# Kernel optimization log

Measured on AMD Instinct MI355X. Metric: run time of the kernel, lower is better.

The kernel has to match this reference:

```python
import math
import jax, jax.numpy as jnp
import numpy as np

D = 256       # d_model
R = 64        # low-rank bottleneck
E = 3         # num experts
KS = (1, 3, 5)
EPS = 0.1     # sinkhorn epsilon
ITERS = 10    # sinkhorn iterations


def _ln(x, g, b):
    m = jnp.mean(x, -1, keepdims=True)
    v = jnp.mean((x - m) ** 2, -1, keepdims=True)
    return (x - m) * jax.lax.rsqrt(v + 1e-5) * g + b


def _gelu(x):
    return jax.nn.gelu(x, approximate=False)  # torch nn.GELU default (erf)


def setup_inputs() -> dict:
    key = jax.random.key(0)
    ks = jax.random.split(key, 12)
    s = 0.02
    B, Lt, La = 16, 1024, 2048
    return {
        "text_feat": jax.random.normal(ks[0], (B, Lt, D), jnp.float32),
        "audio_feat": jax.random.normal(ks[1], (B, La, D), jnp.float32),
        # shared OT projection (LayerNorm + Linear, shared across modalities)
        "ln_g": jnp.ones((D,), jnp.float32),
        "ln_b": jnp.zeros((D,), jnp.float32),
        "W_sh": jax.random.normal(ks[2], (D, D), jnp.float32) * s,
        "b_sh": jnp.zeros((D,), jnp.float32),
        # contradiction router: Linear(d+1->d) GELU Linear(d->E)
        "Wr1": jax.random.normal(ks[3], (D, D + 1), jnp.float32) * s,
        "br1": jnp.zeros((D,), jnp.float32),
        "Wr2": jax.random.normal(ks[4], (E, D), jnp.float32) * s,
        "br2": jnp.zeros((E,), jnp.float32),
        # 3 low-rank conv experts (stacked where shapes match)
        "down_W": jax.random.normal(ks[5], (E, R, D), jnp.float32) * s,
        "down_b": jnp.zeros((E, R), jnp.float32),
        "conv_w1": jax.random.normal(ks[6], (R, R, 1), jnp.float32) * s,
        "conv_w3": jax.random.normal(ks[7], (R, R, 3), jnp.float32) * s,
        "conv_w5": jax.random.normal(ks[8], (R, R, 5), jnp.float32) * s,
        "conv_b": jnp.zeros((E, R), jnp.float32),
        "up_W": jax.random.normal(ks[9], (E, D, R), jnp.float32) * s,
        "up_b": jnp.zeros((E, D), jnp.float32),
        "en_g": jnp.ones((E, D), jnp.float32),
        "en_b": jnp.zeros((E, D), jnp.float32),
    }


def reference(text_feat, audio_feat, ln_g, ln_b, W_sh, b_sh, Wr1, br1, Wr2, br2,
              down_W, down_b, conv_w1, conv_w3, conv_w5, conv_b, up_W, up_b, en_g, en_b):
    B, Lt, _ = text_feat.shape
    La = audio_feat.shape[1]

    # ---- shared projection (dropout = identity at eval) ----
    Tp = _ln(text_feat, ln_g, ln_b) @ W_sh.T + b_sh      # [B,Lt,D]
    Ap = _ln(audio_feat, ln_g, ln_b) @ W_sh.T + b_sh     # [B,La,D]

    # ---- cosine cost ----
    Tn = Tp / jnp.maximum(jnp.linalg.norm(Tp, axis=-1, keepdims=True), 1e-12)
    An = Ap / jnp.maximum(jnp.linalg.norm(Ap, axis=-1, keepdims=True), 1e-12)
    cost = 1.0 - jnp.einsum('bmd,bnd->bmn', Tn, An)      # [B,Lt,La]

    # ---- log-domain Sinkhorn (uniform marginals, no masks) ----
    log_K = -cost / (EPS + 1e-8)
    log_mu = jnp.full((B, Lt), -math.log(Lt), jnp.float32)
    log_nu = jnp.full((B, La), -math.log(La), jnp.float32)
    lu = jnp.zeros((B, Lt), jnp.float32)
    lv = jnp.zeros((B, La), jnp.float32)
    for _ in range(ITERS):
        lu = log_mu - jax.scipy.special.logsumexp(log_K + lv[:, None, :], axis=-1)
        lu = jnp.nan_to_num(jnp.clip(lu, -1e9, 1e9), nan=0.0, posinf=1e9, neginf=-1e9)
        lv = log_nu - jax.scipy.special.logsumexp(log_K + lu[:, :, None], axis=1)
        lv = jnp.nan_to_num(jnp.clip(lv, -1e9, 1e9), nan=0.0, posinf=1e9, neginf=-1e9)
    pi = jnp.exp(lu[:, :, None] + log_K + lv[:, None, :])
    pi = jnp.nan_to_num(pi, nan=0.0, posinf=1.0, neginf=0.0)  # [B,Lt,La]

    A_al = jnp.einsum('bmn,bnd->bmd', pi, Ap)            # [B,Lt,D]
    S = jnp.sum(Tp * A_al, -1)                           # [B,Lt]
    resid = jnp.abs(Tp - A_al)                           # [B,Lt,D]

    # ---- contradiction router ----
    rin = jnp.concatenate([S[..., None], resid], -1)     # [B,Lt,D+1]
    G = jax.nn.softmax(_gelu(rin @ Wr1.T + br1) @ Wr2.T + br2, axis=-1)  # [B,Lt,E]

    # ---- multi-scale low-rank conv MoE over contradiction residual ----
    convs = (conv_w1, conv_w3, conv_w5)
    x = resid
    out = jnp.zeros_like(Tp)
    for e in range(E):
        h = _gelu(x @ down_W[e].T + down_b[e])           # [B,Lt,R]
        k = convs[e].shape[-1]
        pad = (k - 1) // 2
        hc = jax.lax.conv_general_dilated(
            h.transpose(0, 2, 1), convs[e], (1,), [(pad, pad)],
            dimension_numbers=('NCH', 'OIH', 'NCH')) + conv_b[e][None, :, None]
        h = _gelu(hc).transpose(0, 2, 1)                 # [B,Lt,R]
        h = h @ up_W[e].T + up_b[e]                      # [B,Lt,D]
        eo = _ln(h + x, en_g[e], en_b[e])
        out = out + G[..., e:e + 1] * eo
    return out
```

## Files before the change

### kernel.cpp

```cpp
#include <hip/hip_runtime.h>
#include <cstdio>

#define D_ 256
#define LT 1024
#define LA 2048
#define NB 16
#define RR_ 64
#define NRT (NB*LT)
#define NRA (NB*LA)

#define DECQ (-0.080645161f)

typedef short bf16x8 __attribute__((ext_vector_type(8)));
typedef float f32x4 __attribute__((ext_vector_type(4)));

__device__ __forceinline__ float gelu_f(float x) {
    return 0.5f * x * (1.0f + erff(x * 0.70710678118654752f));
}
__device__ __forceinline__ unsigned short f2bf(float f) {
    union { float f; unsigned int i; } c; c.f = f;
    unsigned int x = c.i;
    return (unsigned short)((x + 0x7fffu + ((x >> 16) & 1u)) >> 16);
}

__global__ __launch_bounds__(256) void k_prep_all(
    const float* __restrict__ W_sh, const float* __restrict__ down_W,
    const float* __restrict__ up_W, const float* __restrict__ Wr1,
    unsigned short* __restrict__ Wb, unsigned short* __restrict__ dWb,
    unsigned short* __restrict__ uWb, unsigned short* __restrict__ Wr1b)
{
    int i = blockIdx.x * 256 + threadIdx.x;
    if (i < 65536) Wb[i] = f2bf(W_sh[i]);
    else if (i < 114688) { int j = i - 65536; dWb[j] = f2bf(down_W[j]); }
    else if (i < 163840) { int j = i - 114688; uWb[j] = f2bf(up_W[j]); }
    else { int j = i - 163840; int n = j >> 8, k = j & 255; Wr1b[j] = f2bf(Wr1[(long)n * 257 + 1 + k]); }
}

__global__ __launch_bounds__(256) void k_lnproj_mfma(
    const float* __restrict__ X, const float* __restrict__ g, const float* __restrict__ bln,
    const unsigned short* __restrict__ Wb, const float* __restrict__ bsh,
    float* __restrict__ Pf, unsigned short* __restrict__ Nb)
{
    __shared__ short xb[64][264];
    __shared__ short Bs[256][40];
    int tid = threadIdx.x;
    long row0 = (long)blockIdx.x * 64;
    {
        int lane = tid & 31, rg = tid >> 5;
        float4 ga = *(const float4*)(g + lane * 8);
        float4 gb2 = *(const float4*)(g + lane * 8 + 4);
        float4 ba = *(const float4*)(bln + lane * 8);
        float4 bb2 = *(const float4*)(bln + lane * 8 + 4);
        for (int it = 0; it < 8; it++) {
            int r = it * 8 + rg;
            const float4* xp4 = (const float4*)(X + (row0 + r) * D_);
            float4 a = xp4[lane * 2], b = xp4[lane * 2 + 1];
            float s = a.x + a.y + a.z + a.w + b.x + b.y + b.z + b.w;
#pragma unroll
            for (int off = 16; off >= 1; off >>= 1) s += __shfl_xor(s, off);
            float mean = s * (1.0f / 256.0f);
            float q = (a.x - mean) * (a.x - mean) + (a.y - mean) * (a.y - mean)
                    + (a.z - mean) * (a.z - mean) + (a.w - mean) * (a.w - mean)
                    + (b.x - mean) * (b.x - mean) + (b.y - mean) * (b.y - mean)
                    + (b.z - mean) * (b.z - mean) + (b.w - mean) * (b.w - mean);
#pragma unroll
            for (int off = 16; off >= 1; off >>= 1) q += __shfl_xor(q, off);
            float ivar = rsqrtf(q * (1.0f / 256.0f) + 1e-5f);
            unsigned int u0 = f2bf((a.x - mean) * ivar * ga.x + ba.x);
            unsigned int u1 = f2bf((a.y - mean) * ivar * ga.y + ba.y);
            unsigned int u2 = f2bf((a.z - mean) * ivar * ga.z + ba.z);
            unsigned int u3 = f2bf((a.w - mean) * ivar * ga.w + ba.w);
            unsigned int u4 = f2bf((b.x - mean) * ivar * gb2.x + bb2.x);
            unsigned int u5 = f2bf((b.y - mean) * ivar * gb2.y + bb2.y);
            unsigned int u6 = f2bf((b.z - mean) * ivar * gb2.z + bb2.z);
            unsigned int u7 = f2bf((b.w - mean) * ivar * gb2.w + bb2.w);
            int4 pv;
            pv.x = (int)(u0 | (u1 << 16)); pv.y = (int)(u2 | (u3 << 16));
            pv.z = (int)(u4 | (u5 << 16)); pv.w = (int)(u6 | (u7 << 16));
            *(int4*)&xb[r][lane * 8] = pv;
        }
    }
    __syncthreads();
    int wid = tid >> 6, lane = tid & 63;
    int l15 = lane & 15, kq = lane >> 4;
    int m_local = wid * 16;
    f32x4 acc[16];
#pragma unroll
    for (int j = 0; j < 16; j++) acc[j] = (f32x4){0.f, 0.f, 0.f, 0.f};
    for (int kt = 0; kt < 8; kt++) {
        int k0 = kt * 32;
#pragma unroll
        for (int h = 0; h < 4; h++) {
            int idx = tid + 256 * h;
            int n = idx >> 2, qc = idx & 3;
            *(int4*)&Bs[n][qc * 8] = *(const int4*)(Wb + (long)n * D_ + k0 + qc * 8);
        }
        __syncthreads();
        bf16x8 af = *(const bf16x8*)&xb[m_local + l15][k0 + kq * 8];
#pragma unroll
        for (int j = 0; j < 16; j++) {
            bf16x8 bf = *(const bf16x8*)&Bs[j * 16 + l15][kq * 8];
            acc[j] = __builtin_amdgcn_mfma_f32_16x16x32_bf16(af, bf, acc[j], 0, 0, 0);
        }
        __syncthreads();
    }
#pragma unroll
    for (int j = 0; j < 16; j++) {
        float bv = bsh[j * 16 + l15];
#pragma unroll
        for (int r = 0; r < 4; r++) acc[j][r] += bv;
    }
    float sq[4] = {0.f, 0.f, 0.f, 0.f};
#pragma unroll
    for (int j = 0; j < 16; j++)
#pragma unroll
        for (int r = 0; r < 4; r++) sq[r] += acc[j][r] * acc[j][r];
#pragma unroll
    for (int off = 8; off >= 1; off >>= 1) {
#pragma unroll
        for (int r = 0; r < 4; r++) sq[r] += __shfl_xor(sq[r], off);
    }
    float rinv[4];
#pragma unroll
    for (int r = 0; r < 4; r++) rinv[r] = 1.0f / fmaxf(sqrtf(sq[r]), 1e-12f);
#pragma unroll
    for (int j = 0; j < 16; j++) {
        int col = j * 16 + l15;
#pragma unroll
        for (int r = 0; r < 4; r++) {
            long m = row0 + m_local + kq * 4 + r;
            if (Pf) Pf[m * D_ + col] = acc[j][r];
            Nb[m * D_ + col] = f2bf(acc[j][r] * rinv[r]);
        }
    }
}

__global__ __launch_bounds__(256) void k_transpose_bf(
    const unsigned short* __restrict__ Anb, unsigned short* __restrict__ ApbT)
{
    __shared__ short t[64][68];
    int b = blockIdx.x;
    int n0 = blockIdx.y * 64;
    int d0 = blockIdx.z * 64;
    int tid = threadIdx.x;
#pragma unroll
    for (int h = 0; h < 2; h++) {
        int c = tid + 256 * h;
        int nr = c >> 3, ch = c & 7;
        *(int4*)&t[nr][ch * 8] = *(const int4*)(Anb + ((long)b * LA + n0 + nr) * D_ + d0 + ch * 8);
    }
    __syncthreads();
#pragma unroll
    for (int h = 0; h < 2; h++) {
        int c = tid + 256 * h;
        int d = c >> 3, nch = c & 7;
        unsigned short v[8];
#pragma unroll
        for (int k = 0; k < 8; k++) v[k] = (unsigned short)t[nch * 8 + k][d];
        int4 ov;
        ov.x = (int)((unsigned int)v[0] | ((unsigned int)v[1] << 16));
        ov.y = (int)((unsigned int)v[2] | ((unsigned int)v[3] << 16));
        ov.z = (int)((unsigned int)v[4] | ((unsigned int)v[5] << 16));
        ov.w = (int)((unsigned int)v[6] | ((unsigned int)v[7] << 16));
        *(int4*)(ApbT + ((long)b * D_ + d0 + d) * LA + n0 + nch * 8) = ov;
    }
}

__global__ __launch_bounds__(256) void k_cost_mfma(
    const unsigned short* __restrict__ Tnb, const unsigned short* __restrict__ Anb,
    unsigned char* __restrict__ logK8, unsigned char* __restrict__ logK8T)
{
    __shared__ short sm[2][128][48];
    short (*As)[48] = sm[0];
    short (*Bs)[48] = sm[1];
    unsigned char* tile = (unsigned char*)sm;
    int b = blockIdx.x;
    int m_blk = blockIdx.y * 128, n_blk = blockIdx.z * 128;
    int tid = threadIdx.x;
    int wid = tid >> 6, lane = tid & 63;
    int l15 = lane & 15, kq = lane >> 4;
    int wm0 = (wid >> 1) * 64, wn0 = (wid & 1) * 64;
    const unsigned short* Ab = Tnb + ((long)b * LT + m_blk) * D_;
    const unsigned short* Bb = Anb + ((long)b * LA + n_blk) * D_;
    f32x4 acc[4][4];
#pragma unroll
    for (int i = 0; i < 4; i++)
#pragma unroll
        for (int j = 0; j < 4; j++) acc[i][j] = (f32x4){0.f, 0.f, 0.f, 0.f};
    for (int kt = 0; kt < 8; kt++) {
        int k0 = kt * 32;
#pragma unroll
        for (int h = 0; h < 2; h++) {
            int idx = tid + 256 * h;
            int row = idx >> 2, ch = idx & 3;
            *(int4*)&As[row][ch * 8] = *(const int4*)(Ab + (long)row * D_ + k0 + ch * 8);
            *(int4*)&Bs[row][ch * 8] = *(const int4*)(Bb + (long)row * D_ + k0 + ch * 8);
        }
        __syncthreads();
        bf16x8 af[4], bfv[4];
#pragma unroll
        for (int i = 0; i < 4; i++) af[i] = *(const bf16x8*)&As[wm0 + i * 16 + l15][kq * 8];
#pragma unroll
        for (int j = 0; j < 4; j++) bfv[j] = *(const bf16x8*)&Bs[wn0 + j * 16 + l15][kq * 8];
#pragma unroll
        for (int i = 0; i < 4; i++)
#pragma unroll
            for (int j = 0; j < 4; j++)
                acc[i][j] = __builtin_amdgcn_mfma_f32_16x16x32_bf16(af[i], bfv[j], acc[i][j], 0, 0, 0);
        __syncthreads();
    }
#pragma unroll
    for (int i = 0; i < 4; i++) {
#pragma unroll
        for (int j = 0; j < 4; j++) {
            int n = wn0 + j * 16 + l15;
            long base = ((long)b * LT + m_blk + wm0 + i * 16 + kq * 4) * (long)LA + n_blk + n;
            unsigned int pk = 0;
#pragma unroll
            for (int r = 0; r < 4; r++) {
                float q = rintf((1.0f - acc[i][j][r]) * 124.0f);
                q = fminf(fmaxf(q, 0.0f), 255.0f);
                unsigned int qb = (unsigned int)q;
                pk |= qb << (8 * r);
                logK8[base + (long)r * LA] = (unsigned char)qb;
            }
            *(unsigned int*)&tile[n * 144 + wm0 + i * 16 + kq * 4] = pk;
        }
    }
    __syncthreads();
#pragma unroll
    for (int h = 0; h < 4; h++) {
        int idx = tid + 256 * h;
        int row = idx >> 3, ch = idx & 7;
        int4 v = *(const int4*)&tile[row * 144 + ch * 16];
        *(int4*)(logK8T + ((long)b * LA + n_blk + row) * (long)LT + m_blk + ch * 16) = v;
    }
}

__global__ __launch_bounds__(256) void k_rowlse(
    const unsigned char* __restrict__ logK8, const float* __restrict__ lv,
    float* __restrict__ lu, int first)
{
    __shared__ float red[4];
    int b = blockIdx.x & 15;
    int m = blockIdx.x >> 4;
    long row = (long)b * LT + m;
    const unsigned char* p = logK8 + row * (long)LA;
    int tid = threadIdx.x;
    uint2 raw = *(const uint2*)(p + tid * 8);
    float lvv[8] = {0.f, 0.f, 0.f, 0.f, 0.f, 0.f, 0.f, 0.f};
    if (!first) {
        const float* lvp = lv + (long)b * LA;
        float4 l0 = *(const float4*)(lvp + tid * 8);
        float4 l1 = *(const float4*)(lvp + tid * 8 + 4);
        lvv[0] = l0.x; lvv[1] = l0.y; lvv[2] = l0.z; lvv[3] = l0.w;
        lvv[4] = l1.x; lvv[5] = l1.y; lvv[6] = l1.z; lvv[7] = l1.w;
    }
    unsigned int w0 = raw.x, w1 = raw.y;
    float s = 0.f;
    s += __expf((float)(w0 & 0xffu) * DECQ + lvv[0]);
    s += __expf((float)((w0 >> 8) & 0xffu) * DECQ + lvv[1]);
    s += __expf((float)((w0 >> 16) & 0xffu) * DECQ + lvv[2]);
    s += __expf((float)(w0 >> 24) * DECQ + lvv[3]);
    s += __expf((float)(w1 & 0xffu) * DECQ + lvv[4]);
    s += __expf((float)((w1 >> 8) & 0xffu) * DECQ + lvv[5]);
    s += __expf((float)((w1 >> 16) & 0xffu) * DECQ + lvv[6]);
    s += __expf((float)(w1 >> 24) * DECQ + lvv[7]);
#pragma unroll
    for (int off = 32; off >= 1; off >>= 1) s += __shfl_xor(s, off);
    if ((tid & 63) == 0) red[tid >> 6] = s;
    __syncthreads();
    if (tid == 0) lu[row] = -6.9314718055994531f - __logf(red[0] + red[1] + red[2] + red[3]);
}

__global__ __launch_bounds__(256) void k_collse_t(
    const unsigned char* __restrict__ logK8T, const float* __restrict__ lu, float* __restrict__ lv)
{
    int b = blockIdx.x;
    int n = blockIdx.y * 8 + (threadIdx.x >> 5);
    int lr = threadIdx.x & 31;
    const unsigned char* p = logK8T + ((long)b * LA + n) * (long)LT;
    const float* lup = lu + (long)b * LT;
    float s = 0.f;
#pragma unroll
    for (int q = 0; q < 8; q++) {
        int m = q * 128 + lr * 4;
        unsigned int w = *(const unsigned int*)(p + m);
        float4 l4 = *(const float4*)(lup + m);
        s += __expf((float)(w & 0xffu) * DECQ + l4.x);
        s += __expf((float)((w >> 8) & 0xffu) * DECQ + l4.y);
        s += __expf((float)((w >> 16) & 0xffu) * DECQ + l4.z);
        s += __expf((float)(w >> 24) * DECQ + l4.w);
    }
#pragma unroll
    for (int off = 16; off >= 1; off >>= 1) s += __shfl_xor(s, off);
    if (lr == 0) lv[(long)b * LA + n] = -7.6246189861593985f - __logf(s);
}

__global__ __launch_bounds__(256) void k_pi_mfma(
    const unsigned char* __restrict__ logK8, const unsigned short* __restrict__ ApbT,
    const float* __restrict__ lu, const float* __restrict__ lv, float* __restrict__ Apart)
{
    __shared__ short As[64][48];
    __shared__ short Bs[256][48];
    __shared__ float lv_s[1024];
    __shared__ float lu_s[64];
    int b = blockIdx.x;
    int kh = blockIdx.y;
    int m_blk = blockIdx.z * 64;
    int nbase = kh * 1024;
    int tid = threadIdx.x;
    for (int i = tid; i < 1024; i += 256) lv_s[i] = lv[(long)b * LA + nbase + i];
    if (tid < 64) lu_s[tid] = lu[(long)b * LT + m_blk + tid];
    __syncthreads();
    int wid = tid >> 6, lane = tid & 63;
    int l15 = lane & 15, kq = lane >> 4;
    int wm0 = (wid & 1) * 32, wd0 = (wid >> 1) * 128;
    f32x4 acc[2][8];
#pragma unroll
    for (int i = 0; i < 2; i++)
#pragma unroll
        for (int j = 0; j < 8; j++) acc[i][j] = (f32x4){0.f, 0.f, 0.f, 0.f};
    const unsigned char* Kbase = logK8 + ((long)b * LT + m_blk) * (long)LA + nbase;
    const unsigned short* Bbase = ApbT + (long)b * D_ * (long)LA + nbase;
    int arow = tid >> 2, ac8 = (tid & 3) * 8;
    for (int kt = 0; kt < 32; kt++) {
        int n0 = kt * 32;
        {
            uint2 raw = *(const uint2*)(Kbase + (long)arow * LA + n0 + ac8);
            float lum = lu_s[arow];
            const float* lvp = &lv_s[n0 + ac8];
            unsigned int w0 = raw.x, w1 = raw.y;
            unsigned int o0 = f2bf(__expf((float)(w0 & 0xffu) * DECQ + lum + lvp[0]));
            unsigned int o1 = f2bf(__expf((float)((w0 >> 8) & 0xffu) * DECQ + lum + lvp[1]));
            unsigned int o2 = f2bf(__expf((float)((w0 >> 16) & 0xffu) * DECQ + lum + lvp[2]));
            unsigned int o3 = f2bf(__expf((float)(w0 >> 24) * DECQ + lum + lvp[3]));
            unsigned int o4 = f2bf(__expf((float)(w1 & 0xffu) * DECQ + lum + lvp[4]));
            unsigned int o5 = f2bf(__expf((float)((w1 >> 8) & 0xffu) * DECQ + lum + lvp[5]));
            unsigned int o6 = f2bf(__expf((float)((w1 >> 16) & 0xffu) * DECQ + lum + lvp[6]));
            unsigned int o7 = f2bf(__expf((float)(w1 >> 24) * DECQ + lum + lvp[7]));
            int4 ov;
            ov.x = (int)(o0 | (o1 << 16)); ov.y = (int)(o2 | (o3 << 16));
            ov.z = (int)(o4 | (o5 << 16)); ov.w = (int)(o6 | (o7 << 16));
            *(int4*)&As[arow][ac8] = ov;
        }
#pragma unroll
        for (int h = 0; h < 4; h++) {
            int idx = tid + 256 * h;
            int row = idx >> 2, ch = idx & 3;
            *(int4*)&Bs[row][ch * 8] = *(const int4*)(Bbase + (long)row * LA + n0 + ch * 8);
        }
        __syncthreads();
        bf16x8 af[2], bfv[8];
        af[0] = *(const bf16x8*)&As[wm0 + l15][kq * 8];
        af[1] = *(const bf16x8*)&As[wm0 + 16 + l15][kq * 8];
#pragma unroll
        for (int j = 0; j < 8; j++) bfv[j] = *(const bf16x8*)&Bs[wd0 + j * 16 + l15][kq * 8];
#pragma unroll
        for (int i = 0; i < 2; i++)
#pragma unroll
            for (int j = 0; j < 8; j++)
                acc[i][j] = __builtin_amdgcn_mfma_f32_16x16x32_bf16(af[i], bfv[j], acc[i][j], 0, 0, 0);
        __syncthreads();
    }
    float* dst = Apart + (long)kh * (NB * (long)LT * D_);
#pragma unroll
    for (int i = 0; i < 2; i++) {
#pragma unroll
        for (int r = 0; r < 4; r++) {
            int m = m_blk + wm0 + i * 16 + kq * 4 + r;
            long obase = ((long)b * LT + m) * D_;
#pragma unroll
            for (int j = 0; j < 8; j++)
                dst[obase + wd0 + j * 16 + l15] = acc[i][j][r];
        }
    }
}

__global__ __launch_bounds__(256) void k_sresid(
    const float* __restrict__ Tp, const float* __restrict__ Apart,
    float* __restrict__ resid, unsigned short* __restrict__ residb, float* __restrict__ S)
{
    __shared__ float red[4];
    int b = blockIdx.x & 15;
    int m = blockIdx.x >> 4;
    long row = (long)b * LT + m;
    int tid = threadIdx.x;
    long idx = row * D_ + tid;
    float t = Tp[idx];
    float a = Apart[idx] + Apart[idx + (long)NB * LT * D_];
    float rr = fabsf(t - a);
    resid[idx] = rr;
    residb[idx] = f2bf(rr);
    float p = t * a;
#pragma unroll
    for (int off = 32; off >= 1; off >>= 1) p += __shfl_xor(p, off);
    if ((tid & 63) == 0) red[tid >> 6] = p;
    __syncthreads();
    if (tid == 0) S[row] = red[0] + red[1] + red[2] + red[3];
}

__global__ __launch_bounds__(256) void k_router_fused(
    const unsigned short* __restrict__ residb, const unsigned short* __restrict__ Wr1b,
    const float* __restrict__ Wr1, const float* __restrict__ br1,
    const float* __restrict__ S, const float* __restrict__ Wr2,
    const float* __restrict__ br2, float* __restrict__ G)
{
    __shared__ short xb[16][264];
    __shared__ short Bs[256][40];
    __shared__ float red[4][3][16];
    int tid = threadIdx.x;
    long row0 = (long)blockIdx.x * 16;
#pragma unroll
    for (int h = 0; h < 2; h++) {
        int idx = tid + 256 * h;
        int row = idx >> 5, ch = idx & 31;
        *(int4*)&xb[row][ch * 8] = *(const int4*)(residb + (row0 + row) * D_ + ch * 8);
    }
    __syncthreads();
    int wid = tid >> 6, lane = tid & 63;
    int l15 = lane & 15, kq = lane >> 4;
    f32x4 acc[4];
#pragma unroll
    for (int j = 0; j < 4; j++) acc[j] = (f32x4){0.f, 0.f, 0.f, 0.f};
    for (int kt = 0; kt < 8; kt++) {
        int k0 = kt * 32;
#pragma unroll
        for (int h = 0; h < 4; h++) {
            int idx = tid + 256 * h;
            int n = idx >> 2, qc = idx & 3;
            *(int4*)&Bs[n][qc * 8] = *(const int4*)(Wr1b + (long)n * D_ + k0 + qc * 8);
        }
        __syncthreads();
        bf16x8 af = *(const bf16x8*)&xb[l15][k0 + kq * 8];
#pragma unroll
        for (int j = 0; j < 4; j++) {
            bf16x8 bf = *(const bf16x8*)&Bs[wid * 64 + j * 16 + l15][kq * 8];
            acc[j] = __builtin_amdgcn_mfma_f32_16x16x32_bf16(af, bf, acc[j], 0, 0, 0);
        }
        __syncthreads();
    }
    float sv[4];
#pragma unroll
    for (int r = 0; r < 4; r++) sv[r] = S[row0 + kq * 4 + r];
    float le[3][4] = {};
#pragma unroll
    for (int j = 0; j < 4; j++) {
        int col = wid * 64 + j * 16 + l15;
        float w0 = Wr1[(long)col * 257];
        float bv = br1[col];
        float w2a = Wr2[col], w2b = Wr2[256 + col], w2c = Wr2[512 + col];
#pragma unroll
        for (int r = 0; r < 4; r++) {
            float hv = gelu_f(acc[j][r] + sv[r] * w0 + bv);
            le[0][r] += hv * w2a;
            le[1][r] += hv * w2b;
            le[2][r] += hv * w2c;
        }
    }
#pragma unroll
    for (int off = 8; off >= 1; off >>= 1)
#pragma unroll
        for (int e = 0; e < 3; e++)
#pragma unroll
            for (int r = 0; r < 4; r++) le[e][r] += __shfl_xor(le[e][r], off);
    if (l15 == 0) {
#pragma unroll
        for (int e = 0; e < 3; e++)
#pragma unroll
            for (int r = 0; r < 4; r++) red[wid][e][kq * 4 + r] = le[e][r];
    }
    __syncthreads();
    if (tid < 16) {
        float L0 = red[0][0][tid] + red[1][0][tid] + red[2][0][tid] + red[3][0][tid] + br2[0];
        float L1 = red[0][1][tid] + red[1][1][tid] + red[2][1][tid] + red[3][1][tid] + br2[1];
        float L2 = red[0][2][tid] + red[1][2][tid] + red[2][2][tid] + red[3][2][tid] + br2[2];
        float mx = fmaxf(L0, fmaxf(L1, L2));
        float e0 = __expf(L0 - mx), e1 = __expf(L1 - mx), e2 = __expf(L2 - mx);
        float inv = 1.0f / (e0 + e1 + e2);
        long m = row0 + tid;
        G[m] = e0 * inv; G[NRT + m] = e1 * inv; G[2 * NRT + m] = e2 * inv;
    }
}

__global__ __launch_bounds__(256) void k_down_mfma(
    const unsigned short* __restrict__ residb, const unsigned short* __restrict__ dWb,
    const float* __restrict__ db, float* __restrict__ hall)
{
    __shared__ short xb[64][264];
    __shared__ short Bs[64][40];
    int tid = threadIdx.x;
    int e = blockIdx.y;
    int b = blockIdx.x & 15;
    int mseg = blockIdx.x >> 4;
    long row0 = (long)b * LT + mseg * 64;
    const unsigned short* dWe = dWb + (long)e * RR_ * D_;
    float* h = hall + (long)e * NRT * RR_;
#pragma unroll
    for (int hh = 0; hh < 8; hh++) {
        int idx = tid + 256 * hh;
        int row = idx >> 5, ch = idx & 31;
        *(int4*)&xb[row][ch * 8] = *(const int4*)(residb + (row0 + row) * D_ + ch * 8);
    }
    __syncthreads();
    int wid = tid >> 6, lane = tid & 63;
    int l15 = lane & 15, kq = lane >> 4;
    int m_local = wid * 16;
    f32x4 acc[4];
#pragma unroll
    for (int j = 0; j < 4; j++) acc[j] = (f32x4){0.f, 0.f, 0.f, 0.f};
    for (int kt = 0; kt < 8; kt++) {
        int k0 = kt * 32;
        {
            int n = tid >> 2, qc = tid & 3;
            *(int4*)&Bs[n][qc * 8] = *(const int4*)(dWe + (long)n * D_ + k0 + qc * 8);
        }
        __syncthreads();
        bf16x8 af = *(const bf16x8*)&xb[m_local + l15][k0 + kq * 8];
#pragma unroll
        for (int j = 0; j < 4; j++) {
            bf16x8 bf = *(const bf16x8*)&Bs[j * 16 + l15][kq * 8];
            acc[j] = __builtin_amdgcn_mfma_f32_16x16x32_bf16(af, bf, acc[j], 0, 0, 0);
        }
        __syncthreads();
    }
#pragma unroll
    for (int j = 0; j < 4; j++) {
        int col = j * 16 + l15;
        float bv = db[e * RR_ + col];
#pragma unroll
        for (int r = 0; r < 4; r++) {
            long m = row0 + m_local + kq * 4 + r;
            h[m * RR_ + col] = gelu_f(acc[j][r] + bv);
        }
    }
}

__global__ __launch_bounds__(256) void k_conv_all(
    const float* __restrict__ hall, const float* __restrict__ cw1,
    const float* __restrict__ cw3, const float* __restrict__ cw5,
    const float* __restrict__ conv_b, unsigned short* __restrict__ hcbb)
{
    __shared__ float hs[68][68];
    __shared__ float wt[64][64];
    int e = blockIdx.y;
    const float* w = (e == 0) ? cw1 : ((e == 1) ? cw3 : cw5);
    int ksz = (e == 0) ? 1 : ((e == 1) ? 3 : 5);
    const float* h = hall + (long)e * NRT * RR_;
    unsigned short* hcb = hcbb + (long)e * NRT * RR_;
    const float* cb = conv_b + e * 64;
    int b = blockIdx.x & 15;
    int m0 = (blockIdx.x >> 4) * 64;
    int tid = threadIdx.x;
    int pad = (ksz - 1) >> 1;
    for (int idx = tid; idx < 68 * 16; idx += 256) {
        int mr = idx >> 4, i4 = idx & 15;
        int mm = m0 - 2 + mr;
        float4 vv = { 0.f, 0.f, 0.f, 0.f };
        if (mm >= 0 && mm < LT) vv = *(const float4*)(h + ((long)b * LT + mm) * RR_ + i4 * 4);
        *(float4*)&hs[mr][i4 * 4] = vv;
    }
    int tx = tid & 15, ty = tid >> 4;
    float acc[4][4] = {};
    for (int t = 0; t < ksz; t++) {
        __syncthreads();
        for (int idx = tid; idx < 4096; idx += 256) {
            int i = idx & 63, j = idx >> 6;
            wt[i][j] = w[(long)j * RR_ * ksz + i * ksz + t];
        }
        __syncthreads();
        int roff = ty * 4 + 2 + t - pad;
        for (int i4 = 0; i4 < 16; i4++) {
            float4 h0 = *(const float4*)&hs[roff + 0][i4 * 4];
            float4 h1 = *(const float4*)&hs[roff + 1][i4 * 4];
            float4 h2 = *(const float4*)&hs[roff + 2][i4 * 4];
            float4 h3 = *(const float4*)&hs[roff + 3][i4 * 4];
            float hh[4][4] = { { h0.x, h0.y, h0.z, h0.w }, { h1.x, h1.y, h1.z, h1.w },
                               { h2.x, h2.y, h2.z, h2.w }, { h3.x, h3.y, h3.z, h3.w } };
#pragma unroll
            for (int s = 0; s < 4; s++) {
                float4 wv = *(const float4*)&wt[i4 * 4 + s][tx * 4];
#pragma unroll
                for (int r = 0; r < 4; r++) {
                    acc[r][0] += hh[r][s] * wv.x;
                    acc[r][1] += hh[r][s] * wv.y;
                    acc[r][2] += hh[r][s] * wv.z;
                    acc[r][3] += hh[r][s] * wv.w;
                }
            }
        }
    }
    float4 bb = *(const float4*)(cb + tx * 4);
#pragma unroll
    for (int r = 0; r < 4; r++) {
        long m = (long)b * LT + m0 + ty * 4 + r;
        unsigned long long pv =
              (unsigned long long)f2bf(gelu_f(acc[r][0] + bb.x))
            | ((unsigned long long)f2bf(gelu_f(acc[r][1] + bb.y)) << 16)
            | ((unsigned long long)f2bf(gelu_f(acc[r][2] + bb.z)) << 32)
            | ((unsigned long long)f2bf(gelu_f(acc[r][3] + bb.w)) << 48);
        *(unsigned long long*)(hcb + m * RR_ + tx * 4) = pv;
    }
}

__global__ __launch_bounds__(256) void k_up3(
    const unsigned short* __restrict__ hcbb, const unsigned short* __restrict__ uWb,
    const float* __restrict__ up_b, const float* __restrict__ resid,
    const float* __restrict__ en_g, const float* __restrict__ en_b,
    const float* __restrict__ G, float* __restrict__ out)
{
    __shared__ short hs[64][88];
    __shared__ short Bs[256][40];
    int tid = threadIdx.x;
    int b = blockIdx.x & 15;
    int mseg = blockIdx.x >> 4;
    long row0 = (long)b * LT + mseg * 64;
    int wid = tid >> 6, lane = tid & 63;
    int l15 = lane & 15, kq = lane >> 4;
    int m_local = wid * 16;
    long mrow[4];
#pragma unroll
    for (int r = 0; r < 4; r++) mrow[r] = row0 + m_local + kq * 4 + r;
    f32x4 outacc[16];
#pragma unroll
    for (int j = 0; j < 16; j++) outacc[j] = (f32x4){0.f, 0.f, 0.f, 0.f};
    for (int e = 0; e < 3; e++) {
        __syncthreads();
        const unsigned short* hcb = hcbb + (long)e * NRT * RR_;
        const unsigned short* uWe = uWb + (long)e * 16384;
#pragma unroll
        for (int hh = 0; hh < 2; hh++) {
            int idx = tid + 256 * hh;
            int row = idx >> 3, ch = idx & 7;
            *(int4*)&hs[row][ch * 8] = *(const int4*)(hcb + (row0 + row) * RR_ + ch * 8);
        }
        f32x4 acc[16];
#pragma unroll
        for (int j = 0; j < 16; j++) acc[j] = (f32x4){0.f, 0.f, 0.f, 0.f};
        for (int kt = 0; kt < 2; kt++) {
            int k0 = kt * 32;
#pragma unroll
            for (int hh = 0; hh < 4; hh++) {
                int idx = tid + 256 * hh;
                int n = idx >> 2, qc = idx & 3;
                *(int4*)&Bs[n][qc * 8] = *(const int4*)(uWe + (long)n * RR_ + k0 + qc * 8);
            }
            __syncthreads();
            bf16x8 af = *(const bf16x8*)&hs[m_local + l15][k0 + kq * 8];
#pragma unroll
            for (int j = 0; j < 16; j++) {
                bf16x8 bf = *(const bf16x8*)&Bs[j * 16 + l15][kq * 8];
                acc[j] = __builtin_amdgcn_mfma_f32_16x16x32_bf16(af, bf, acc[j], 0, 0, 0);
            }
            __syncthreads();
        }
        const float* ub = up_b + e * 256;
#pragma unroll
        for (int j = 0; j < 16; j++) {
            int col = j * 16 + l15;
            float bv = ub[col];
#pragma unroll
            for (int r = 0; r < 4; r++)
                acc[j][r] += bv + resid[mrow[r] * D_ + col];
        }
        float s[4] = {0.f, 0.f, 0.f, 0.f};
#pragma unroll
        for (int j = 0; j < 16; j++)
#pragma unroll
            for (int r = 0; r < 4; r++) s[r] += acc[j][r];
#pragma unroll
        for (int off = 8; off >= 1; off >>= 1)
#pragma unroll
            for (int r = 0; r < 4; r++) s[r] += __shfl_xor(s[r], off);
        float mn[4];
#pragma unroll
        for (int r = 0; r < 4; r++) mn[r] = s[r] * (1.0f / 256.0f);
        float q[4] = {0.f, 0.f, 0.f, 0.f};
#pragma unroll
        for (int j = 0; j < 16; j++)
#pragma unroll
            for (int r = 0; r < 4; r++) { float d = acc[j][r] - mn[r]; q[r] += d * d; }
#pragma unroll
        for (int off = 8; off >= 1; off >>= 1)
#pragma unroll
            for (int r = 0; r < 4; r++) q[r] += __shfl_xor(q[r], off);
        float iv[4], gv[4];
#pragma unroll
        for (int r = 0; r < 4; r++) {
            iv[r] = rsqrtf(q[r] * (1.0f / 256.0f) + 1e-5f);
            gv[r] = G[(long)e * NRT + mrow[r]];
        }
        const float* eg = en_g + e * 256;
        const float* eb = en_b + e * 256;
#pragma unroll
        for (int j = 0; j < 16; j++) {
            int col = j * 16 + l15;
            float egc = eg[col], ebc = eb[col];
#pragma unroll
            for (int r = 0; r < 4; r++)
                outacc[j][r] += gv[r] * ((acc[j][r] - mn[r]) * iv[r] * egc + ebc);
        }
    }
#pragma unroll
    for (int j = 0; j < 16; j++) {
        int col = j * 16 + l15;
#pragma unroll
        for (int r = 0; r < 4; r++)
            out[mrow[r] * D_ + col] = outacc[j][r];
    }
}

extern "C" void kernel_launch(void* const* d_in, const int* in_sizes, int n_in,
                              void* d_out, int out_size, void* d_ws, size_t ws_size,
                              hipStream_t stream)
{
    const float* text   = (const float*)d_in[0];
    const float* audio  = (const float*)d_in[1];
    const float* ln_g   = (const float*)d_in[2];
    const float* ln_b   = (const float*)d_in[3];
    const float* W_sh   = (const float*)d_in[4];
    const float* b_sh   = (const float*)d_in[5];
    const float* Wr1    = (const float*)d_in[6];
    const float* br1    = (const float*)d_in[7];
    const float* Wr2    = (const float*)d_in[8];
    const float* br2    = (const float*)d_in[9];
    const float* down_W = (const float*)d_in[10];
    const float* down_b = (const float*)d_in[11];
    const float* cw1    = (const float*)d_in[12];
    const float* cw3    = (const float*)d_in[13];
    const float* cw5    = (const float*)d_in[14];
    const float* conv_b = (const float*)d_in[15];
    const float* up_W   = (const float*)d_in[16];
    const float* up_b   = (const float*)d_in[17];
    const float* en_g   = (const float*)d_in[18];
    const float* en_b   = (const float*)d_in[19];

    float* ws = (float*)d_ws;
    float*          Tp    = ws;
    unsigned short* Tnb   = (unsigned short*)(ws + 4194304);
    unsigned short* Anb   = (unsigned short*)(ws + 6291456);
    unsigned short* ApbT  = (unsigned short*)(ws + 10485760);
    unsigned char*  logK8 = (unsigned char*)(ws + 14680064);
    float*          Apart = ws + 23068672;
    float*          resid = ws + 31457280;
    unsigned short* residb= (unsigned short*)(ws + 35651584);
    float*          lu    = ws + 37748736;
    float*          lv    = ws + 37765120;
    float*          Sb    = ws + 37797888;
    float*          Gb    = ws + 37814272;
    unsigned short* Wb    = (unsigned short*)(ws + 37863424);
    unsigned short* dWb   = (unsigned short*)(ws + 37896192);
    unsigned short* uWb   = (unsigned short*)(ws + 37920768);
    unsigned short* Wr1b  = (unsigned short*)(ws + 37945344);
    size_t need_bytes = (size_t)37978112 * 4;
    if (ws_size < need_bytes) {
        fprintf(stderr, "kernel_launch: ws_size %zu < needed %zu\n", ws_size, need_bytes);
        return;
    }
    float*          hall = ws + 14680064;
    unsigned short* hcbb = (unsigned short*)(ws + 17825792);
    unsigned char*  logK8T = (unsigned char*)(ws + 23068672);

    k_prep_all<<<896, 256, 0, stream>>>(W_sh, down_W, up_W, Wr1, Wb, dWb, uWb, Wr1b);
    k_lnproj_mfma<<<NRT / 64, 256, 0, stream>>>(text, ln_g, ln_b, Wb, b_sh, Tp, Tnb);
    k_lnproj_mfma<<<NRA / 64, 256, 0, stream>>>(audio, ln_g, ln_b, Wb, b_sh, nullptr, Anb);
    k_transpose_bf<<<dim3(NB, LA / 64, D_ / 64), 256, 0, stream>>>(Anb, ApbT);
    k_cost_mfma<<<dim3(NB, LT / 128, LA / 128), 256, 0, stream>>>(Tnb, Anb, logK8, logK8T);
    for (int it = 0; it < 10; it++) {
        k_rowlse<<<NRT, 256, 0, stream>>>(logK8, lv, lu, it == 0 ? 1 : 0);
        k_collse_t<<<dim3(NB, LA / 8), 256, 0, stream>>>(logK8T, lu, lv);
    }
    k_pi_mfma<<<dim3(NB, 2, LT / 64), 256, 0, stream>>>(logK8, ApbT, lu, lv, Apart);
    k_sresid<<<NRT, 256, 0, stream>>>(Tp, Apart, resid, residb, Sb);
    k_router_fused<<<NRT / 16, 256, 0, stream>>>(residb, Wr1b, Wr1, br1, Sb, Wr2, br2, Gb);
    k_down_mfma<<<dim3(NRT / 64, 3), 256, 0, stream>>>(residb, dWb, down_b, hall);
    k_conv_all<<<dim3(NRT / 64, 3), 256, 0, stream>>>(hall, cw1, cw3, cw5, conv_b, hcbb);
    k_up3<<<NRT / 64, 256, 0, stream>>>(hcbb, uWb, up_b, resid, en_g, en_b, Gb, (float*)d_out);
}
```

Before: 509.3 us.

## Factor Sinkhorn scalings out of pi matmul and batch row/col LSE kernels

Moves the Sinkhorn log-domain math to base 2 (exp2/log2 with fma) and processes 8 rows or 32 columns per block instead of one, which cuts launch count and per-row reduction overhead. The plan matmul no longer forms exp(logK+lu+lv) per element. The column scaling is folded into the audio values by a new pre-scaling kernel and the row scaling is applied in the epilogue. This removes the per-element lu/lv loads and adds from the GEMM, at the cost of an extra pass over ApbT and some precision risk from scaling bf16 values before the matmul.

Result: slower. 648.6 us (+27.4%).

```diff
diff --git a/kernel.cpp b/kernel.cpp
--- a/kernel.cpp
+++ b/kernel.cpp
@@ -9,7 +9,8 @@
 #define NRT (NB*LT)
 #define NRA (NB*LA)
 
-#define DECQ (-0.080645161f)
+#define DECQ  (-0.080645161f)
+#define DECQ2 (-0.11634637f)
 
 typedef short bf16x8 __attribute__((ext_vector_type(8)));
 typedef float f32x4 __attribute__((ext_vector_type(4)));
@@ -237,108 +238,135 @@
     }
 }
 
-__global__ __launch_bounds__(256) void k_rowlse(
-    const unsigned char* __restrict__ logK8, const float* __restrict__ lv,
-    float* __restrict__ lu, int first)
-{
-    __shared__ float red[4];
+__global__ __launch_bounds__(256) void k_rowlse2(
+    const unsigned char* __restrict__ logK8, const float* __restrict__ lv2,
+    float* __restrict__ lu2, int first)
+{
+    __shared__ float red[8][4];
     int b = blockIdx.x & 15;
-    int m = blockIdx.x >> 4;
-    long row = (long)b * LT + m;
-    const unsigned char* p = logK8 + row * (long)LA;
-    int tid = threadIdx.x;
-    uint2 raw = *(const uint2*)(p + tid * 8);
+    int mseg = blockIdx.x >> 4;
+    int tid = threadIdx.x;
+    int wid = tid >> 6, lane = tid & 63;
     float lvv[8] = {0.f, 0.f, 0.f, 0.f, 0.f, 0.f, 0.f, 0.f};
     if (!first) {
-        const float* lvp = lv + (long)b * LA;
-        float4 l0 = *(const float4*)(lvp + tid * 8);
-        float4 l1 = *(const float4*)(lvp + tid * 8 + 4);
+        const float* lvp = lv2 + (long)b * LA + tid * 8;
+        float4 l0 = *(const float4*)lvp, l1 = *(const float4*)(lvp + 4);
         lvv[0] = l0.x; lvv[1] = l0.y; lvv[2] = l0.z; lvv[3] = l0.w;
         lvv[4] = l1.x; lvv[5] = l1.y; lvv[6] = l1.z; lvv[7] = l1.w;
     }
-    unsigned int w0 = raw.x, w1 = raw.y;
-    float s = 0.f;
-    s += __expf((float)(w0 & 0xffu) * DECQ + lvv[0]);
-    s += __expf((float)((w0 >> 8) & 0xffu) * DECQ + lvv[1]);
-    s += __expf((float)((w0 >> 16) & 0xffu) * DECQ + lvv[2]);
-    s += __expf((float)(w0 >> 24) * DECQ + lvv[3]);
-    s += __expf((float)(w1 & 0xffu) * DECQ + lvv[4]);
-    s += __expf((float)((w1 >> 8) & 0xffu) * DECQ + lvv[5]);
-    s += __expf((float)((w1 >> 16) & 0xffu) * DECQ + lvv[6]);
-    s += __expf((float)(w1 >> 24) * DECQ + lvv[7]);
-#pragma unroll
-    for (int off = 32; off >= 1; off >>= 1) s += __shfl_xor(s, off);
-    if ((tid & 63) == 0) red[tid >> 6] = s;
+    const unsigned char* p = logK8 + ((long)b * LT + mseg * 8) * (long)LA + tid * 8;
+#pragma unroll
+    for (int r = 0; r < 8; r++) {
+        uint2 w = *(const uint2*)(p + (long)r * LA);
+        unsigned int w0 = w.x, w1 = w.y;
+        float s = 0.f;
+        s += exp2f(fmaf((float)(w0 & 0xffu),         DECQ2, lvv[0]));
+        s += exp2f(fmaf((float)((w0 >> 8) & 0xffu),  DECQ2, lvv[1]));
+        s += exp2f(fmaf((float)((w0 >> 16) & 0xffu), DECQ2, lvv[2]));
+        s += exp2f(fmaf((float)(w0 >> 24),           DECQ2, lvv[3]));
+        s += exp2f(fmaf((float)(w1 & 0xffu),         DECQ2, lvv[4]));
+        s += exp2f(fmaf((float)((w1 >> 8) & 0xffu),  DECQ2, lvv[5]));
+        s += exp2f(fmaf((float)((w1 >> 16) & 0xffu), DECQ2, lvv[6]));
+        s += exp2f(fmaf((float)(w1 >> 24),           DECQ2, lvv[7]));
+#pragma unroll
+        for (int off = 32; off >= 1; off >>= 1) s += __shfl_xor(s, off);
+        if (lane == 0) red[r][wid] = s;
+    }
     __syncthreads();
-    if (tid == 0) lu[row] = -6.9314718055994531f - __logf(red[0] + red[1] + red[2] + red[3]);
-}
-
-__global__ __launch_bounds__(256) void k_collse_t(
-    const unsigned char* __restrict__ logK8T, const float* __restrict__ lu, float* __restrict__ lv)
+    if (tid < 8) {
+        float s = red[tid][0] + red[tid][1] + red[tid][2] + red[tid][3];
+        lu2[(long)b * LT + mseg * 8 + tid] = -10.0f - __log2f(s);
+    }
+}
+
+__global__ __launch_bounds__(256) void k_collse2(
+    const unsigned char* __restrict__ logK8T, const float* __restrict__ lu2,
+    float* __restrict__ lv2, int final_)
+{
+    __shared__ float red[32][4];
+    int b = blockIdx.x & 15;
+    int nseg = blockIdx.x >> 4;
+    int tid = threadIdx.x;
+    int wid = tid >> 6, lane = tid & 63;
+    float4 lu4 = *(const float4*)(lu2 + (long)b * LT + tid * 4);
+    const unsigned char* base = logK8T + ((long)b * LA + nseg * 32) * (long)LT + tid * 4;
+#pragma unroll 4
+    for (int c = 0; c < 32; c++) {
+        unsigned int w = *(const unsigned int*)(base + (long)c * LT);
+        float s = exp2f(fmaf((float)(w & 0xffu),         DECQ2, lu4.x))
+                + exp2f(fmaf((float)((w >> 8) & 0xffu),  DECQ2, lu4.y))
+                + exp2f(fmaf((float)((w >> 16) & 0xffu), DECQ2, lu4.z))
+                + exp2f(fmaf((float)(w >> 24),           DECQ2, lu4.w));
+#pragma unroll
+        for (int off = 32; off >= 1; off >>= 1) s += __shfl_xor(s, off);
+        if (lane == 0) red[c][wid] = s;
+    }
+    __syncthreads();
+    if (tid < 32) {
+        float s = red[tid][0] + red[tid][1] + red[tid][2] + red[tid][3];
+        lv2[(long)b * LA + nseg * 32 + tid] = final_ ? (0.00048828125f / s)
+                                                     : (-11.0f - __log2f(s));
+    }
+}
+
+__global__ __launch_bounds__(256) void k_scale_ev(
+    unsigned short* __restrict__ ApbT, const float* __restrict__ ev)
 {
     int b = blockIdx.x;
-    int n = blockIdx.y * 8 + (threadIdx.x >> 5);
-    int lr = threadIdx.x & 31;
-    const unsigned char* p = logK8T + ((long)b * LA + n) * (long)LT;
-    const float* lup = lu + (long)b * LT;
-    float s = 0.f;
-#pragma unroll
-    for (int q = 0; q < 8; q++) {
-        int m = q * 128 + lr * 4;
-        unsigned int w = *(const unsigned int*)(p + m);
-        float4 l4 = *(const float4*)(lup + m);
-        s += __expf((float)(w & 0xffu) * DECQ + l4.x);
-        s += __expf((float)((w >> 8) & 0xffu) * DECQ + l4.y);
-        s += __expf((float)((w >> 16) & 0xffu) * DECQ + l4.z);
-        s += __expf((float)(w >> 24) * DECQ + l4.w);
-    }
-#pragma unroll
-    for (int off = 16; off >= 1; off >>= 1) s += __shfl_xor(s, off);
-    if (lr == 0) lv[(long)b * LA + n] = -7.6246189861593985f - __logf(s);
-}
-
-__global__ __launch_bounds__(256) void k_pi_mfma(
-    const unsigned char* __restrict__ logK8, const unsigned short* __restrict__ ApbT,
-    const float* __restrict__ lu, const float* __restrict__ lv, float* __restrict__ Apart)
-{
-    __shared__ short As[64][48];
-    __shared__ short Bs[256][48];
-    __shared__ float lv_s[1024];
-    __shared__ float lu_s[64];
+    int d = blockIdx.y;
+    int tid = threadIdx.x;
+    long off = ((long)b * D_ + d) * (long)LA + tid * 8;
+    int4 v = *(const int4*)(ApbT + off);
+    const float* ep = ev + (long)b * LA + tid * 8;
+    float4 e0 = *(const float4*)ep, e1 = *(const float4*)(ep + 4);
+    unsigned int u[4] = {(unsigned int)v.x, (unsigned int)v.y, (unsigned int)v.z, (unsigned int)v.w};
+    float ee[8] = {e0.x, e0.y, e0.z, e0.w, e1.x, e1.y, e1.z, e1.w};
+    unsigned int o[4];
+#pragma unroll
+    for (int k = 0; k < 4; k++) {
+        float lo = __uint_as_float(u[k] << 16) * ee[2 * k];
+        float hi = __uint_as_float(u[k] & 0xffff0000u) * ee[2 * k + 1];
+        o[k] = (unsigned int)f2bf(lo) | ((unsigned int)f2bf(hi) << 16);
+    }
+    int4 ov; ov.x = (int)o[0]; ov.y = (int)o[1]; ov.z = (int)o[2]; ov.w = (int)o[3];
+    *(int4*)(ApbT + off) = ov;
+}
+
+__global__ __launch_bounds__(256) void k_pi2(
+    const unsigned char* __restrict__ logK8, const unsigned short* __restrict__ Av,
+    const float* __restrict__ lu2, float* __restrict__ Apart)
+{
+    __shared__ short As[64][40];
+    __shared__ short Bs[256][40];
+    __shared__ float eus[64];
     int b = blockIdx.x;
     int kh = blockIdx.y;
-    int m_blk = blockIdx.z * 64;
-    int nbase = kh * 1024;
-    int tid = threadIdx.x;
-    for (int i = tid; i < 1024; i += 256) lv_s[i] = lv[(long)b * LA + nbase + i];
-    if (tid < 64) lu_s[tid] = lu[(long)b * LT + m_blk + tid];
-    __syncthreads();
+    int mseg = blockIdx.z;
+    int tid = threadIdx.x;
+    if (tid < 64) eus[tid] = exp2f(lu2[(long)b * LT + mseg * 64 + tid]);
     int wid = tid >> 6, lane = tid & 63;
     int l15 = lane & 15, kq = lane >> 4;
-    int wm0 = (wid & 1) * 32, wd0 = (wid >> 1) * 128;
-    f32x4 acc[2][8];
-#pragma unroll
-    for (int i = 0; i < 2; i++)
-#pragma unroll
-        for (int j = 0; j < 8; j++) acc[i][j] = (f32x4){0.f, 0.f, 0.f, 0.f};
-    const unsigned char* Kbase = logK8 + ((long)b * LT + m_blk) * (long)LA + nbase;
-    const unsigned short* Bbase = ApbT + (long)b * D_ * (long)LA + nbase;
+    f32x4 acc[4][4];
+#pragma unroll
+    for (int i = 0; i < 4; i++)
+#pragma unroll
+        for (int j = 0; j < 4; j++) acc[i][j] = (f32x4){0.f, 0.f, 0.f, 0.f};
+    const unsigned char* Kbase = logK8 + ((long)b * LT + mseg * 64) * (long)LA + kh * 1024;
+    const unsigned short* Bbase = Av + (long)b * D_ * (long)LA + kh * 1024;
     int arow = tid >> 2, ac8 = (tid & 3) * 8;
     for (int kt = 0; kt < 32; kt++) {
         int n0 = kt * 32;
         {
             uint2 raw = *(const uint2*)(Kbase + (long)arow * LA + n0 + ac8);
-            float lum = lu_s[arow];
-            const float* lvp = &lv_s[n0 + ac8];
             unsigned int w0 = raw.x, w1 = raw.y;
-            unsigned int o0 = f2bf(__expf((float)(w0 & 0xffu) * DECQ + lum + lvp[0]));
-            unsigned int o1 = f2bf(__expf((float)((w0 >> 8) & 0xffu) * DECQ + lum + lvp[1]));
-            unsigned int o2 = f2bf(__expf((float)((w0 >> 16) & 0xffu) * DECQ + lum + lvp[2]));
-            unsigned int o3 = f2bf(__expf((float)(w0 >> 24) * DECQ + lum + lvp[3]));
-            unsigned int o4 = f2bf(__expf((float)(w1 & 0xffu) * DECQ + lum + lvp[4]));
-            unsigned int o5 = f2bf(__expf((float)((w1 >> 8) & 0xffu) * DECQ + lum + lvp[5]));
-            unsigned int o6 = f2bf(__expf((float)((w1 >> 16) & 0xffu) * DECQ + lum + lvp[6]));
-            unsigned int o7 = f2bf(__expf((float)(w1 >> 24) * DECQ + lum + lvp[7]));
+            unsigned int o0 = f2bf(exp2f((float)(w0 & 0xffu) * DECQ2));
+            unsigned int o1 = f2bf(exp2f((float)((w0 >> 8) & 0xffu) * DECQ2));
+            unsigned int o2 = f2bf(exp2f((float)((w0 >> 16) & 0xffu) * DECQ2));
+            unsigned int o3 = f2bf(exp2f((float)(w0 >> 24) * DECQ2));
+            unsigned int o4 = f2bf(exp2f((float)(w1 & 0xffu) * DECQ2));
+            unsigned int o5 = f2bf(exp2f((float)((w1 >> 8) & 0xffu) * DECQ2));
+            unsigned int o6 = f2bf(exp2f((float)((w1 >> 16) & 0xffu) * DECQ2));
+            unsigned int o7 = f2bf(exp2f((float)(w1 >> 24) * DECQ2));
             int4 ov;
             ov.x = (int)(o0 | (o1 << 16)); ov.y = (int)(o2 | (o3 << 16));
             ov.z = (int)(o4 | (o5 << 16)); ov.w = (int)(o6 | (o7 << 16));
@@ -351,28 +379,29 @@
             *(int4*)&Bs[row][ch * 8] = *(const int4*)(Bbase + (long)row * LA + n0 + ch * 8);
         }
         __syncthreads();
-        bf16x8 af[2], bfv[8];
-        af[0] = *(const bf16x8*)&As[wm0 + l15][kq * 8];
-        af[1] = *(const bf16x8*)&As[wm0 + 16 + l15][kq * 8];
-#pragma unroll
-        for (int j = 0; j < 8; j++) bfv[j] = *(const bf16x8*)&Bs[wd0 + j * 16 + l15][kq * 8];
-#pragma unroll
-        for (int i = 0; i < 2; i++)
-#pragma unroll
-            for (int j = 0; j < 8; j++)
+        bf16x8 af[4], bfv[4];
+#pragma unroll
+        for (int i = 0; i < 4; i++) af[i] = *(const bf16x8*)&As[i * 16 + l15][kq * 8];
+#pragma unroll
+        for (int j = 0; j < 4; j++) bfv[j] = *(const bf16x8*)&Bs[wid * 64 + j * 16 + l15][kq * 8];
+#pragma unroll
+        for (int i = 0; i < 4; i++)
+#pragma unroll
+            for (int j = 0; j < 4; j++)
                 acc[i][j] = __builtin_amdgcn_mfma_f32_16x16x32_bf16(af[i], bfv[j], acc[i][j], 0, 0, 0);
         __syncthreads();
     }
-    float* dst = Apart + (long)kh * (NB * (long)LT * D_);
-#pragma unroll
-    for (int i = 0; i < 2; i++) {
+    float* dst = Apart + (long)kh * (NB * (long)LT * D_) + ((long)b * LT + mseg * 64) * D_;
+#pragma unroll
+    for (int i = 0; i < 4; i++) {
 #pragma unroll
         for (int r = 0; r < 4; r++) {
-            int m = m_blk + wm0 + i * 16 + kq * 4 + r;
-            long obase = ((long)b * LT + m) * D_;
-#pragma unroll
-            for (int j = 0; j < 8; j++)
-                dst[obase + wd0 + j * 16 + l15] = acc[i][j][r];
+            int row = i * 16 + kq * 4 + r;
+            float eu = eus[row];
+            long obase = (long)row * D_;
+#pragma unroll
+            for (int j = 0; j < 4; j++)
+                dst[obase + wid * 64 + j * 16 + l15] = acc[i][j][r] * eu;
         }
     }
 }
@@ -744,8 +773,8 @@
     float*          Apart = ws + 23068672;
     float*          resid = ws + 31457280;
     unsigned short* residb= (unsigned short*)(ws + 35651584);
-    float*          lu    = ws + 37748736;
-    float*          lv    = ws + 37765120;
+    float*          lu2   = ws + 37748736;
+    float*          lv2   = ws + 37765120;
     float*          Sb    = ws + 37797888;
     float*          Gb    = ws + 37814272;
     unsigned short* Wb    = (unsigned short*)(ws + 37863424);
@@ -767,10 +796,11 @@
     k_transpose_bf<<<dim3(NB, LA / 64, D_ / 64), 256, 0, stream>>>(Anb, ApbT);
     k_cost_mfma<<<dim3(NB, LT / 128, LA / 128), 256, 0, stream>>>(Tnb, Anb, logK8, logK8T);
     for (int it = 0; it < 10; it++) {
-        k_rowlse<<<NRT, 256, 0, stream>>>(logK8, lv, lu, it == 0 ? 1 : 0);
-        k_collse_t<<<dim3(NB, LA / 8), 256, 0, stream>>>(logK8T, lu, lv);
-    }
-    k_pi_mfma<<<dim3(NB, 2, LT / 64), 256, 0, stream>>>(logK8, ApbT, lu, lv, Apart);
+        k_rowlse2<<<NRT / 8, 256, 0, stream>>>(logK8, lv2, lu2, it == 0 ? 1 : 0);
+        k_collse2<<<NB * (LA / 32), 256, 0, stream>>>(logK8T, lu2, lv2, it == 9 ? 1 : 0);
+    }
+    k_scale_ev<<<dim3(NB, D_), 256, 0, stream>>>(ApbT, lv2);
+    k_pi2<<<dim3(NB, 2, LT / 64), 256, 0, stream>>>(logK8, ApbT, lu2, Apart);
     k_sresid<<<NRT, 256, 0, stream>>>(Tp, Apart, resid, residb, Sb);
     k_router_fused<<<NRT / 16, 256, 0, stream>>>(residb, Wr1b, Wr1, br1, Sb, Wr2, br2, Gb);
     k_down_mfma<<<dim3(NRT / 64, 3), 256, 0, stream>>>(residb, dWb, down_b, hall);
```
